# Kernel optimization log

Measured on AMD Instinct MI355X. Metric: run time of the kernel, lower is better.

The kernel has to match this reference:

```python
import jax, jax.numpy as jnp
import numpy as np

BATCH = 4096
IN_F = 1024
OUT_F = 1024
GRID_SIZE = 8
SPLINE_ORDER = 3
SCALE_SPLINE = 1.0


def setup_inputs() -> dict:
    key = jax.random.key(0)
    kx, kb, ks = jax.random.split(key, 3)
    # inputs live on the spline domain [-1, 1]
    x = jax.random.uniform(kx, (BATCH, IN_F), jnp.float32, -1.0, 1.0)
    # kaiming_uniform_(a=sqrt(5)) on (out,in) -> U(-1/sqrt(in), 1/sqrt(in))
    bound = 1.0 / float(np.sqrt(IN_F))
    base_weight = jax.random.uniform(kb, (OUT_F, IN_F), jnp.float32, -bound, bound)
    # normal(mean=0, std=0.1), (out, in, grid_size + spline_order)
    spline_weight = 0.1 * jax.random.normal(ks, (OUT_F, IN_F, GRID_SIZE + SPLINE_ORDER), jnp.float32)
    # uniform knot vector with spacing h = 2/grid_size over [-1,1], extended by
    # spline_order knots on each side so Cox-de Boor yields grid_size+spline_order bases
    h = 2.0 / GRID_SIZE
    grid = jnp.arange(-SPLINE_ORDER, GRID_SIZE + SPLINE_ORDER + 1, dtype=jnp.float32) * h - 1.0
    return {"x": x, "base_weight": base_weight, "spline_weight": spline_weight, "grid": grid}


def b_spline_basis(x, grid, k):
    # x: (batch, in), grid: (grid_size + 2k + 1,) shared across (out, in) pairs
    xe = x[..., None]  # (b, i, 1)
    # degree-0: indicator of knot interval -> (b, i, grid_size + 2k)
    basis = ((xe >= grid[:-1]) & (xe < grid[1:])).astype(x.dtype)
    for d in range(1, k + 1):  # Cox-de Boor recursion up to degree k
        left_denom = grid[d:-1] - grid[:-(d + 1)]
        right_denom = grid[d + 1:] - grid[1:-d]
        left_denom = jnp.where(left_denom > 0, left_denom, 1.0)
        right_denom = jnp.where(right_denom > 0, right_denom, 1.0)
        basis = ((xe - grid[:-(d + 1)]) / left_denom * basis[..., :-1]
                 + (grid[d + 1:] - xe) / right_denom * basis[..., 1:])
    return basis  # (b, i, grid_size + k)


def reference(x, base_weight, spline_weight, grid):
    base_output = x @ base_weight.T  # (b, out)
    basis = b_spline_basis(x, grid, SPLINE_ORDER)  # (b, i, L), L = grid_size + k
    # grid is identical for every (out, in) pair, so the per-(o,i) basis of the
    # original collapses to a per-i basis; einsum 'bil,oil->bo' is the same math.
    spline_output = jnp.einsum('bil,oil->bo', basis, spline_weight)
    return base_output + SCALE_SPLINE * spline_output
```

## Files before the change

### kernel.cpp

```cpp
#include <hip/hip_runtime.h>
#include <hip/hip_bf16.h>
#include <cstdint>

#define BATCH 4096
#define INF   1024
#define OUTF  1024
#define LCH   12
#define KTOT  (INF*LCH)
#define BM    256
#define BN    256
#define BK    48
#define NT    64
#define THREADS 512
#define TSZ   (6*256*8)

#define WTT_BYTES ((size_t)OUTF * KTOT * 2)
#define PART_FLOATS ((size_t)BATCH * OUTF)
#define PQ_U32   (PART_FLOATS / 2)
#define P_BYTES  ((size_t)4 * PQ_U32 * 4)
#define OUT_BYTES (PART_FLOATS * 4)

typedef __bf16 bf16x8 __attribute__((ext_vector_type(8)));
typedef float  f32x16 __attribute__((ext_vector_type(16)));
typedef unsigned long long ull;
typedef unsigned short us;

struct alignas(16) U2 { ull x, y; };

__device__ __forceinline__ us f2bf(float f) {
  unsigned int u = __builtin_bit_cast(unsigned int, f);
  u += 0x7FFFu + ((u >> 16) & 1u);
  return (us)(u >> 16);
}

__device__ __forceinline__ void async_copy16(const void* g, void* l) {
  __builtin_amdgcn_global_load_lds(
      (const __attribute__((address_space(1))) unsigned int*)g,
      (__attribute__((address_space(3))) unsigned int*)l,
      16, 0, 0);
}

#define PIPE_BARRIER() do {                                        \
  asm volatile("s_waitcnt vmcnt(4) lgkmcnt(0)" ::: "memory");      \
  __builtin_amdgcn_sched_barrier(0);                               \
  __builtin_amdgcn_s_barrier();                                    \
  __builtin_amdgcn_sched_barrier(0);                               \
} while (0)

__device__ __forceinline__ void basis12(float xx, ull W[3]) {
  float u  = fmaf(xx, 4.0f, 7.0f);
  float fm = floorf(u);
  int   mi = (int)fm;
  float t  = u - fm;
  float s  = 1.0f - t;
  float t2 = t * t, t3 = t2 * t;
  float w0 = (s * s * s) * (1.0f / 6.0f);
  float w3 = t3 * (1.0f / 6.0f);
  float w1 = fmaf(0.5f, t3, 2.0f / 3.0f) - t2;
  float w2 = 1.0f - w0 - w1 - w3;
  int ls = mi - 3;
  ull W64 = (ull)f2bf(w0)
          | ((ull)f2bf(w1) << 16)
          | ((ull)f2bf(w2) << 32)
          | ((ull)f2bf(w3) << 48);
  int sh = ls << 4;
  int a  = sh & 63;
  ull lop  = W64 << a;
  ull hip_ = a ? (W64 >> (64 - a)) : 0ull;
  W[0] = (sh < 64) ? lop : 0ull;
  W[1] = (sh < 64) ? hip_ : lop;
  W[2] = ((sh < 64) ? 0ull : hip_) | ((ull)f2bf(xx) << 48);
}

__global__ __launch_bounds__(256) void kan_build_wtT(
    const float* __restrict__ sw,
    const float* __restrict__ bw,
    us* __restrict__ WtT)
{
  int t   = blockIdx.x * 256 + threadIdx.x;
  int col = t & 255;
  int q   = t >> 8;
  int fp  = q & 1;
  int ktG = (q >> 1) & 255;
  int bn  = q >> 9;
  int o   = bn * 256 + col;
  int i0  = ktG * 4 + fp * 2;

  const float2* s2 = reinterpret_cast<const float2*>(
      sw + (size_t)(o * 1024 + i0) * 11);
  float2 sv[11];
#pragma unroll
  for (int l = 0; l < 11; ++l) sv[l] = s2[l];
  float2 bv = *reinterpret_cast<const float2*>(bw + (size_t)o * 1024 + i0);

  us v[24];
#pragma unroll
  for (int l = 0; l < 11; ++l) {
    int m0 = l;
    int m1 = 11 + l;
    float f0 = (m0 & 1) ? sv[m0 >> 1].y : sv[m0 >> 1].x;
    float f1 = (m1 & 1) ? sv[m1 >> 1].y : sv[m1 >> 1].x;
    v[l]      = f2bf(f0);
    v[12 + l] = f2bf(f1);
  }
  v[11] = f2bf(bv.x);
  v[23] = f2bf(bv.y);

  int g0 = fp * 3;
  us* base = WtT + (size_t)(bn * 256 + ktG) * (6 * 256 * 8);
  U2* p = reinterpret_cast<U2*>(base);
#pragma unroll
  for (int j = 0; j < 3; ++j) {
    U2 u;
    const us* w = v + j * 8;
    u.x = (ull)w[0] | ((ull)w[1] << 16) | ((ull)w[2] << 32) | ((ull)w[3] << 48);
    u.y = (ull)w[4] | ((ull)w[5] << 16) | ((ull)w[6] << 32) | ((ull)w[7] << 48);
    p[(g0 + j) * 256 + col] = u;
  }
}

#define BASIS2(XV, W0_,W1_,W2_,W3_,W4_,W5_) do {                         \
  {                                                                      \
    float xx = (XV).x;                                                   \
    float u_  = fmaf(xx, 4.0f, 7.0f);                                    \
    float fm_ = floorf(u_);                                              \
    int   mi_ = (int)fm_;                                                \
    float t_  = u_ - fm_;                                                \
    float s_  = 1.0f - t_;                                               \
    float t2_ = t_ * t_, t3_ = t2_ * t_;                                 \
    float w0_ = (s_ * s_ * s_) * (1.0f / 6.0f);                          \
    float w3_ = t3_ * (1.0f / 6.0f);                                     \
    float w1_ = fmaf(0.5f, t3_, 2.0f / 3.0f) - t2_;                      \
    float w2_ = 1.0f - w0_ - w1_ - w3_;                                  \
    unsigned int p01_, p23_;                                             \
    asm("v_cvt_pk_bf16_f32 %0, %1, %2" : "=v"(p01_) : "v"(w0_), "v"(w1_)); \
    asm("v_cvt_pk_bf16_f32 %0, %1, %2" : "=v"(p23_) : "v"(w2_), "v"(w3_)); \
    ull W64_ = (ull)p01_ | ((ull)p23_ << 32);                            \
    int sh_ = (mi_ - 3) << 4;                                            \
    int a_  = sh_ & 63;                                                  \
    ull lo_ = W64_ << a_;                                                \
    ull hi_ = a_ ? (W64_ >> (64 - a_)) : 0ull;                           \
    W0_ = (sh_ < 64) ? lo_ : 0ull;                                       \
    W1_ = (sh_ < 64) ? hi_ : lo_;                                        \
    W2_ = ((sh_ < 64) ? 0ull : hi_) | ((ull)f2bf(xx) << 48);             \
  }                                                                      \
  {                                                                      \
    float xx = (XV).y;                                                   \
    float u_  = fmaf(xx, 4.0f, 7.0f);                                    \
    float fm_ = floorf(u_);                                              \
    int   mi_ = (int)fm_;                                                \
    float t_  = u_ - fm_;                                                \
    float s_  = 1.0f - t_;                                               \
    float t2_ = t_ * t_, t3_ = t2_ * t_;                                 \
    float w0_ = (s_ * s_ * s_) * (1.0f / 6.0f);                          \
    float w3_ = t3_ * (1.0f / 6.0f);                                     \
    float w1_ = fmaf(0.5f, t3_, 2.0f / 3.0f) - t2_;                      \
    float w2_ = 1.0f - w0_ - w1_ - w3_;                                  \
    unsigned int p01_, p23_;                                             \
    asm("v_cvt_pk_bf16_f32 %0, %1, %2" : "=v"(p01_) : "v"(w0_), "v"(w1_)); \
    asm("v_cvt_pk_bf16_f32 %0, %1, %2" : "=v"(p23_) : "v"(w2_), "v"(w3_)); \
    ull W64_ = (ull)p01_ | ((ull)p23_ << 32);                            \
    int sh_ = (mi_ - 3) << 4;                                            \
    int a_  = sh_ & 63;                                                  \
    ull lo_ = W64_ << a_;                                                \
    ull hi_ = a_ ? (W64_ >> (64 - a_)) : 0ull;                           \
    W3_ = (sh_ < 64) ? lo_ : 0ull;                                       \
    W4_ = (sh_ < 64) ? hi_ : lo_;                                        \
    W5_ = ((sh_ < 64) ? 0ull : hi_) | ((ull)f2bf(xx) << 48);             \
  }                                                                      \
} while (0)

__global__ __launch_bounds__(THREADS, 2) void kan_gemm(
    const float* __restrict__ x,
    const us* __restrict__ WtT,
    unsigned int* __restrict__ P)
{
  __shared__ alignas(16) us smem[5 * TSZ];

  const int tid  = threadIdx.x;
  const int lane = tid & 63;
  const int wid  = tid >> 6;
  const int wm   = (wid >> 2) * 128;
  const int wn   = (wid & 3) * 64;
  const int lo   = lane & 31;
  const int lh   = lane >> 5;
  const int b    = (int)blockIdx.x;
  const int bn   = b & 3;
  const int kq   = (b >> 2) & 3;
  const int bm   = b >> 4;

  const int r   = tid & 255;
  const int fp  = tid >> 8;
  const int g0A = fp * 3;
  const float* xrow = x + (size_t)(bm * BM + r) * INF + kq * 256 + fp * 2;

  us* Acur = smem;
  us* Aalt = smem + TSZ;
  us* Bcur = smem + 2 * TSZ;
  us* Bnxt = smem + 3 * TSZ;
  us* Bnn  = smem + 4 * TSZ;

  f32x16 acc[4][2] = {};

  auto stageB = [&](int c, us* Bd) {
    const int ktG = kq * NT + c;
    const us* base = WtT + (size_t)(bn * 256 + ktG) * (6 * 256 * 8);
#pragma unroll
    for (int j = 0; j < 3; ++j) {
      int s = wid * 3 + j;
      int g = s >> 2, h = s & 3;
      async_copy16(base + g * 2048 + h * 512 + lane * 8,
                   Bd + g * 2048 + h * 512);
    }
  };

#define WRITEW(AD, W0_,W1_,W2_,W3_,W4_,W5_) do {                   \
    U2* p_ = reinterpret_cast<U2*>(AD);                            \
    U2 u0_; u0_.x = W0_; u0_.y = W1_;                              \
    U2 u1_; u1_.x = W2_; u1_.y = W3_;                              \
    U2 u2_; u2_.x = W4_; u2_.y = W5_;                              \
    p_[(g0A + 0) * 256 + r] = u0_;                                 \
    p_[(g0A + 1) * 256 + r] = u1_;                                 \
    p_[(g0A + 2) * 256 + r] = u2_;                                 \
  } while (0)

#define READK(S, A0,A1,A2,A3,B0,B1) do {                           \
    const int kk_ = (S) * 2 + lh;                                  \
    A0 = *reinterpret_cast<const bf16x8*>(&Acur[(kk_ * 256 + wm +  0 + lo) * 8]); \
    A1 = *reinterpret_cast<const bf16x8*>(&Acur[(kk_ * 256 + wm + 32 + lo) * 8]); \
    A2 = *reinterpret_cast<const bf16x8*>(&Acur[(kk_ * 256 + wm + 64 + lo) * 8]); \
    A3 = *reinterpret_cast<const bf16x8*>(&Acur[(kk_ * 256 + wm + 96 + lo) * 8]); \
    B0 = *reinterpret_cast<const bf16x8*>(&Bcur[(kk_ * 256 + wn +  0 + lo) * 8]); \
    B1 = *reinterpret_cast<const bf16x8*>(&Bcur[(kk_ * 256 + wn + 32 + lo) * 8]); \
  } while (0)

#define MFMAK(A0,A1,A2,A3,B0,B1) do {                              \
    acc[0][0] = __builtin_amdgcn_mfma_f32_32x32x16_bf16(A0, B0, acc[0][0], 0, 0, 0); \
    acc[0][1] = __builtin_amdgcn_mfma_f32_32x32x16_bf16(A0, B1, acc[0][1], 0, 0, 0); \
    acc[1][0] = __builtin_amdgcn_mfma_f32_32x32x16_bf16(A1, B0, acc[1][0], 0, 0, 0); \
    acc[1][1] = __builtin_amdgcn_mfma_f32_32x32x16_bf16(A1, B1, acc[1][1], 0, 0, 0); \
    acc[2][0] = __builtin_amdgcn_mfma_f32_32x32x16_bf16(A2, B0, acc[2][0], 0, 0, 0); \
    acc[2][1] = __builtin_amdgcn_mfma_f32_32x32x16_bf16(A2, B1, acc[2][1], 0, 0, 0); \
    acc[3][0] = __builtin_amdgcn_mfma_f32_32x32x16_bf16(A3, B0, acc[3][0], 0, 0, 0); \
    acc[3][1] = __builtin_amdgcn_mfma_f32_32x32x16_bf16(A3, B1, acc[3][1], 0, 0, 0); \
  } while (0)

  {
    float2 x0 = *reinterpret_cast<const float2*>(xrow);
    ull W0, W1, W2, W3, W4, W5;
    BASIS2(x0, W0, W1, W2, W3, W4, W5);
    WRITEW(Acur, W0, W1, W2, W3, W4, W5);
    stageB(0, Bcur);
    stageB(1, Bnxt);
  }
  float2 xa = *reinterpret_cast<const float2*>(xrow + 4);
  PIPE_BARRIER();

  for (int c = 0; c < NT; ++c) {
    const int cf = (c + 2 < NT) ? (c + 2) : (NT - 1);

    float2 xb = *reinterpret_cast<const float2*>(xrow + cf * 4);
    stageB(cf, Bnn);

    ull W0, W1, W2, W3, W4, W5;
    bf16x8 a00, a01, a02, a03, b00, b01;
    bf16x8 a10, a11, a12, a13, b10, b11;
    bf16x8 a20, a21, a22, a23, b20, b21;

    READK(0, a00, a01, a02, a03, b00, b01);
    BASIS2(xa, W0, W1, W2, W3, W4, W5);
    READK(1, a10, a11, a12, a13, b10, b11);
    MFMAK(a00, a01, a02, a03, b00, b01);
    READK(2, a20, a21, a22, a23, b20, b21);
    MFMAK(a10, a11, a12, a13, b10, b11);
    __builtin_amdgcn_sched_barrier(0);
    WRITEW(Aalt, W0, W1, W2, W3, W4, W5);
    MFMAK(a20, a21, a22, a23, b20, b21);

    PIPE_BARRIER();

    us* t = Bcur; Bcur = Bnxt; Bnxt = Bnn; Bnn = t;
    t = Acur; Acur = Aalt; Aalt = t;
    xa = xb;
  }

  asm volatile("s_waitcnt vmcnt(0) lgkmcnt(0)" ::: "memory");

  unsigned int* dst = P + (size_t)kq * PQ_U32;
  const int ubase = bn * 128 + (wn >> 1) + lo;
#pragma unroll
  for (int f = 0; f < 4; ++f) {
#pragma unroll
    for (int rr = 0; rr < 16; ++rr) {
      int row = bm * BM + wm + f * 32 + (rr & 3) + 8 * (rr >> 2) + 4 * lh;
      unsigned int pk;
      asm("v_cvt_pk_bf16_f32 %0, %1, %2"
          : "=v"(pk) : "v"(acc[f][0][rr]), "v"(acc[f][1][rr]));
      dst[(size_t)row * 512 + ubase] = pk;
    }
  }
}

__global__ __launch_bounds__(256) void kan_reduce4p(
    float* __restrict__ out, const uint4* __restrict__ P)
{
  size_t i = (size_t)blockIdx.x * 256 + threadIdx.x;
  const size_t Q = PQ_U32 / 4;
  uint4 a = P[i], b = P[i + Q], c = P[i + 2 * Q], d = P[i + 3 * Q];

  size_t u0  = i * 4;
  size_t row = u0 >> 9;
  int ur  = (int)(u0 & 511);
  int pq  = ur >> 7;
  int sub = (ur >> 5) & 3;
  int lo0 = ur & 31;
  int col0 = pq * 256 + sub * 64 + lo0;

  float4 vlo, vhi;
  {
    unsigned int ua[4] = {a.x, a.y, a.z, a.w};
    unsigned int ub[4] = {b.x, b.y, b.z, b.w};
    unsigned int uc[4] = {c.x, c.y, c.z, c.w};
    unsigned int ud[4] = {d.x, d.y, d.z, d.w};
    float* plo = &vlo.x;
    float* phi = &vhi.x;
#pragma unroll
    for (int j = 0; j < 4; ++j) {
      float la = __builtin_bit_cast(float, ua[j] << 16);
      float lb = __builtin_bit_cast(float, ub[j] << 16);
      float lc = __builtin_bit_cast(float, uc[j] << 16);
      float ld = __builtin_bit_cast(float, ud[j] << 16);
      float ha = __builtin_bit_cast(float, ua[j] & 0xffff0000u);
      float hb = __builtin_bit_cast(float, ub[j] & 0xffff0000u);
      float hc = __builtin_bit_cast(float, uc[j] & 0xffff0000u);
      float hd = __builtin_bit_cast(float, ud[j] & 0xffff0000u);
      plo[j] = (la + lb) + (lc + ld);
      phi[j] = (ha + hb) + (hc + hd);
    }
  }
  *reinterpret_cast<float4*>(out + row * 1024 + col0)      = vlo;
  *reinterpret_cast<float4*>(out + row * 1024 + col0 + 32) = vhi;
}

#define FB_BUFSZ (6*128*8)

__global__ __launch_bounds__(256) void kan_build_wt(
    const float* __restrict__ sw, const float* __restrict__ bw,
    us* __restrict__ Wt)
{
  int idx = blockIdx.x * 256 + threadIdx.x;
  int o = idx >> 10;
  int i = idx & 1023;
  const float* s = sw + (size_t)(o * 1024 + i) * 11;
  us v[12];
#pragma unroll
  for (int l = 0; l < 11; ++l) v[l] = f2bf(s[l]);
  v[11] = f2bf(bw[o * 1024 + i]);
  us* d = Wt + (size_t)o * KTOT + i * 12;
  *reinterpret_cast<ushort4*>(d + 0) = make_ushort4(v[0], v[1], v[2],  v[3]);
  *reinterpret_cast<ushort4*>(d + 4) = make_ushort4(v[4], v[5], v[6],  v[7]);
  *reinterpret_cast<ushort4*>(d + 8) = make_ushort4(v[8], v[9], v[10], v[11]);
}

__global__ __launch_bounds__(512, 4) void kan_gemm_fb(
    const float* __restrict__ x, const us* __restrict__ Wt,
    float* __restrict__ out)
{
  __shared__ alignas(16) us smem[5 * FB_BUFSZ];
  const int tid  = threadIdx.x;
  const int lane = tid & 63;
  const int wid  = tid >> 6;
  const int wm   = (wid >> 2) * 64;
  const int wn   = (wid & 3) * 32;
  const int lo   = lane & 31;
  const int lh   = lane >> 5;
  const int idx  = (int)blockIdx.x;
  const int bn   = idx & 7;
  const int kh   = (idx >> 3) & 1;
  const int bm   = idx >> 4;
  const bool builder = (tid < 256);
  const bool stager  = (wid >= 4);
  const int ab  = tid & 127;
  const int ai0 = ((tid >> 7) & 1) << 1;
  const float* xrow = x + (size_t)(bm * 128 + ab) * INF + kh * 512 + ai0;
  const size_t kbase = (size_t)kh * (KTOT / 2);

  us* Bcur = smem;            us* Bnxt = smem + FB_BUFSZ;
  us* Bnn  = smem + 2 * FB_BUFSZ;
  us* Acur = smem + 3 * FB_BUFSZ; us* Aalt = smem + 4 * FB_BUFSZ;
  f32x16 acc[2] = {};

  auto stageB = [&](int c, us* Bd) {
    const int wq = wid - 4;
#pragma unroll
    for (int qq = 0; qq < 3; ++qq) {
      int G  = (wq * 3 + qq) * 64 + lane;
      int kk = G >> 7;
      int oo = G & 127;
      const us* src = Wt + (size_t)(bn * 128 + oo) * KTOT + kbase + c * 48 + kk * 8;
      async_copy16(src, Bd + (wq * 3 + qq) * 512);
    }
  };
  auto buildA = [&](float2 xv, us* Ad) {
    ull W[6];
    basis12(xv.x, W + 0);
    basis12(xv.y, W + 3);
    U2* p = reinterpret_cast<U2*>(Ad);
    const int g0 = (ai0 >> 1) * 3;
    U2 u0; u0.x = W[0]; u0.y = W[1];
    U2 u1; u1.x = W[2]; u1.y = W[3];
    U2 u2; u2.x = W[4]; u2.y = W[5];
    p[(g0 + 0) * 128 + ab] = u0;
    p[(g0 + 1) * 128 + ab] = u1;
    p[(g0 + 2) * 128 + ab] = u2;
  };

  float2 xa = make_float2(0.f, 0.f);
  if (builder) {
    float2 x0v = *reinterpret_cast<const float2*>(xrow);
    buildA(x0v, Acur);
    xa = *reinterpret_cast<const float2*>(xrow + 4);
  }
  if (stager) { stageB(0, Bcur); stageB(1, Bnxt); }
  asm volatile("s_waitcnt vmcnt(3) lgkmcnt(0)" ::: "memory");
  __builtin_amdgcn_s_barrier();

  for (int c = 0; c < 128; ++c) {
    int cf = (c + 2 < 128) ? (c + 2) : 127;
    float2 xb = xa;
    if (builder) {
      xb = *reinterpret_cast<const float2*>(xrow + cf * 4);
      buildA(xa, Aalt);
    }
    if (stager) stageB(cf, Bnn);
#pragma unroll
    for (int s = 0; s < 3; ++s) {
      const int kk = s * 2 + lh;
      bf16x8 a0 = *reinterpret_cast<const bf16x8*>(&Acur[(kk * 128 + wm + lo) * 8]);
      bf16x8 a1 = *reinterpret_cast<const bf16x8*>(&Acur[(kk * 128 + wm + 32 + lo) * 8]);
      bf16x8 b0 = *reinterpret_cast<const bf16x8*>(&Bcur[(kk * 128 + wn + lo) * 8]);
      acc[0] = __builtin_amdgcn_mfma_f32_32x32x16_bf16(a0, b0, acc[0], 0, 0, 0);
      acc[1] = __builtin_amdgcn_mfma_f32_32x32x16_bf16(a1, b0, acc[1], 0, 0, 0);
    }
    asm volatile("s_waitcnt vmcnt(3) lgkmcnt(0)" ::: "memory");
    __builtin_amdgcn_s_barrier();
    us* t = Bcur; Bcur = Bnxt; Bnxt = Bnn; Bnn = t;
    t = Acur; Acur = Aalt; Aalt = t;
    xa = xb;
  }
  asm volatile("s_waitcnt vmcnt(0) lgkmcnt(0)" ::: "memory");
#pragma unroll
  for (int mf = 0; mf < 2; ++mf)
#pragma unroll
    for (int r2 = 0; r2 < 16; ++r2) {
      int row = bm * 128 + wm + mf * 32 + (r2 & 3) + 8 * (r2 >> 2) + 4 * lh;
      atomicAdd(out + (size_t)row * OUTF + bn * 128 + wn + lo, acc[mf][r2]);
    }
}

extern "C" void kernel_launch(void* const* d_in, const int* in_sizes, int n_in,
                              void* d_out, int out_size, void* d_ws, size_t ws_size,
                              hipStream_t stream) {
  const float* x  = (const float*)d_in[0];
  const float* bw = (const float*)d_in[1];
  const float* sw = (const float*)d_in[2];
  float* out = (float*)d_out;

  if (ws_size >= WTT_BYTES + P_BYTES) {
    us* WtT = (us*)d_ws;
    unsigned int* P = (unsigned int*)((char*)d_ws + WTT_BYTES);
    kan_build_wtT<<<2048, 256, 0, stream>>>(sw, bw, WtT);
    kan_gemm<<<256, THREADS, 0, stream>>>(x, WtT, P);
    kan_reduce4p<<<(int)(PQ_U32 / 4 / 256), 256, 0, stream>>>(
        out, (const uint4*)P);
  } else if (ws_size >= WTT_BYTES) {
    us* Wt = (us*)d_ws;
    kan_build_wt<<<(OUTF * INF) / 256, 256, 0, stream>>>(sw, bw, Wt);
    hipMemsetAsync(d_out, 0, OUT_BYTES, stream);
    kan_gemm_fb<<<512, 512, 0, stream>>>(x, Wt, out);
  }
}
```

Before: 146.6 us.

## Halve GEMM N-tile to 128 and double-buffer B to raise occupancy

Shrinks the GEMM block tile from 256x256 to 256x128 and the per-wave tile to 64x64. B staging drops from triple to double buffering, which cuts LDS and accumulator registers and lets four blocks per CU be requested. The grid doubles to 512 blocks, with the weight pre-layout and reduce column mapping updated to match. In exchange, the spline basis for each A tile is now computed twice (once per N-half), B-tile loads are issued only one step ahead, and each loaded A element gets less reuse.

```diff
diff --git a/kernel.cpp b/kernel.cpp
--- a/kernel.cpp
+++ b/kernel.cpp
@@ -8,11 +8,12 @@
 #define LCH   12
 #define KTOT  (INF*LCH)
 #define BM    256
-#define BN    256
+#define BN    128
 #define BK    48
 #define NT    64
 #define THREADS 512
-#define TSZ   (6*256*8)
+#define ASZ   (6*256*8)
+#define BSZ   (6*128*8)
 
 #define WTT_BYTES ((size_t)OUTF * KTOT * 2)
 #define PART_FLOATS ((size_t)BATCH * OUTF)
@@ -41,7 +42,7 @@
 }
 
 #define PIPE_BARRIER() do {                                        \
-  asm volatile("s_waitcnt vmcnt(4) lgkmcnt(0)" ::: "memory");      \
+  asm volatile("s_waitcnt vmcnt(1) lgkmcnt(0)" ::: "memory");      \
   __builtin_amdgcn_sched_barrier(0);                               \
   __builtin_amdgcn_s_barrier();                                    \
   __builtin_amdgcn_sched_barrier(0);                               \
@@ -78,12 +79,12 @@
     us* __restrict__ WtT)
 {
   int t   = blockIdx.x * 256 + threadIdx.x;
-  int col = t & 255;
-  int q   = t >> 8;
+  int col = t & 127;
+  int q   = t >> 7;
   int fp  = q & 1;
   int ktG = (q >> 1) & 255;
   int bn  = q >> 9;
-  int o   = bn * 256 + col;
+  int o   = bn * 128 + col;
   int i0  = ktG * 4 + fp * 2;
 
   const float2* s2 = reinterpret_cast<const float2*>(
@@ -107,7 +108,7 @@
   v[23] = f2bf(bv.y);
 
   int g0 = fp * 3;
-  us* base = WtT + (size_t)(bn * 256 + ktG) * (6 * 256 * 8);
+  us* base = WtT + (size_t)(bn * 256 + ktG) * (6 * 128 * 8);
   U2* p = reinterpret_cast<U2*>(base);
 #pragma unroll
   for (int j = 0; j < 3; ++j) {
@@ -115,7 +116,7 @@
     const us* w = v + j * 8;
     u.x = (ull)w[0] | ((ull)w[1] << 16) | ((ull)w[2] << 32) | ((ull)w[3] << 48);
     u.y = (ull)w[4] | ((ull)w[5] << 16) | ((ull)w[6] << 32) | ((ull)w[7] << 48);
-    p[(g0 + j) * 256 + col] = u;
+    p[(g0 + j) * 128 + col] = u;
   }
 }
 
@@ -170,24 +171,24 @@
   }                                                                      \
 } while (0)
 
-__global__ __launch_bounds__(THREADS, 2) void kan_gemm(
+__global__ __launch_bounds__(THREADS, 4) void kan_gemm(
     const float* __restrict__ x,
     const us* __restrict__ WtT,
     unsigned int* __restrict__ P)
 {
-  __shared__ alignas(16) us smem[5 * TSZ];
+  __shared__ alignas(16) us smem[2 * ASZ + 2 * BSZ];
 
   const int tid  = threadIdx.x;
   const int lane = tid & 63;
   const int wid  = tid >> 6;
-  const int wm   = (wid >> 2) * 128;
-  const int wn   = (wid & 3) * 64;
+  const int wm   = (wid >> 1) * 64;
+  const int wn   = (wid & 1) * 64;
   const int lo   = lane & 31;
   const int lh   = lane >> 5;
   const int b    = (int)blockIdx.x;
-  const int bn   = b & 3;
-  const int kq   = (b >> 2) & 3;
-  const int bm   = b >> 4;
+  const int bn   = b & 7;
+  const int kq   = (b >> 3) & 3;
+  const int bm   = b >> 5;
 
   const int r   = tid & 255;
   const int fp  = tid >> 8;
@@ -195,22 +196,23 @@
   const float* xrow = x + (size_t)(bm * BM + r) * INF + kq * 256 + fp * 2;
 
   us* Acur = smem;
-  us* Aalt = smem + TSZ;
-  us* Bcur = smem + 2 * TSZ;
-  us* Bnxt = smem + 3 * TSZ;
-  us* Bnn  = smem + 4 * TSZ;
-
-  f32x16 acc[4][2] = {};
+  us* Aalt = smem + ASZ;
+  us* Bcur = smem + 2 * ASZ;
+  us* Balt = smem + 2 * ASZ + BSZ;
+
+  f32x16 acc[2][2] = {};
 
   auto stageB = [&](int c, us* Bd) {
-    const int ktG = kq * NT + c;
-    const us* base = WtT + (size_t)(bn * 256 + ktG) * (6 * 256 * 8);
-#pragma unroll
-    for (int j = 0; j < 3; ++j) {
-      int s = wid * 3 + j;
-      int g = s >> 2, h = s & 3;
-      async_copy16(base + g * 2048 + h * 512 + lane * 8,
-                   Bd + g * 2048 + h * 512);
+    if (wid < 6) {
+      const int ktG = kq * NT + c;
+      const us* base = WtT + (size_t)(bn * 256 + ktG) * (6 * 128 * 8);
+#pragma unroll
+      for (int j = 0; j < 2; ++j) {
+        int ch = wid * 2 + j;
+        int g = ch >> 1, h = ch & 1;
+        async_copy16(base + g * 1024 + h * 512 + lane * 8,
+                     Bd + g * 1024 + h * 512);
+      }
     }
   };
 
@@ -224,34 +226,27 @@
     p_[(g0A + 2) * 256 + r] = u2_;                                 \
   } while (0)
 
-#define READK(S, A0,A1,A2,A3,B0,B1) do {                           \
+#define READK(S, A0,A1,B0,B1) do {                                 \
     const int kk_ = (S) * 2 + lh;                                  \
     A0 = *reinterpret_cast<const bf16x8*>(&Acur[(kk_ * 256 + wm +  0 + lo) * 8]); \
     A1 = *reinterpret_cast<const bf16x8*>(&Acur[(kk_ * 256 + wm + 32 + lo) * 8]); \
-    A2 = *reinterpret_cast<const bf16x8*>(&Acur[(kk_ * 256 + wm + 64 + lo) * 8]); \
-    A3 = *reinterpret_cast<const bf16x8*>(&Acur[(kk_ * 256 + wm + 96 + lo) * 8]); \
-    B0 = *reinterpret_cast<const bf16x8*>(&Bcur[(kk_ * 256 + wn +  0 + lo) * 8]); \
-    B1 = *reinterpret_cast<const bf16x8*>(&Bcur[(kk_ * 256 + wn + 32 + lo) * 8]); \
+    B0 = *reinterpret_cast<const bf16x8*>(&Bcur[(kk_ * 128 + wn +  0 + lo) * 8]); \
+    B1 = *reinterpret_cast<const bf16x8*>(&Bcur[(kk_ * 128 + wn + 32 + lo) * 8]); \
   } while (0)
 
-#define MFMAK(A0,A1,A2,A3,B0,B1) do {                              \
+#define MFMAK(A0,A1,B0,B1) do {                                    \
     acc[0][0] = __builtin_amdgcn_mfma_f32_32x32x16_bf16(A0, B0, acc[0][0], 0, 0, 0); \
     acc[0][1] = __builtin_amdgcn_mfma_f32_32x32x16_bf16(A0, B1, acc[0][1], 0, 0, 0); \
     acc[1][0] = __builtin_amdgcn_mfma_f32_32x32x16_bf16(A1, B0, acc[1][0], 0, 0, 0); \
     acc[1][1] = __builtin_amdgcn_mfma_f32_32x32x16_bf16(A1, B1, acc[1][1], 0, 0, 0); \
-    acc[2][0] = __builtin_amdgcn_mfma_f32_32x32x16_bf16(A2, B0, acc[2][0], 0, 0, 0); \
-    acc[2][1] = __builtin_amdgcn_mfma_f32_32x32x16_bf16(A2, B1, acc[2][1], 0, 0, 0); \
-    acc[3][0] = __builtin_amdgcn_mfma_f32_32x32x16_bf16(A3, B0, acc[3][0], 0, 0, 0); \
-    acc[3][1] = __builtin_amdgcn_mfma_f32_32x32x16_bf16(A3, B1, acc[3][1], 0, 0, 0); \
   } while (0)
 
+  stageB(0, Bcur);
   {
     float2 x0 = *reinterpret_cast<const float2*>(xrow);
     ull W0, W1, W2, W3, W4, W5;
     BASIS2(x0, W0, W1, W2, W3, W4, W5);
     WRITEW(Acur, W0, W1, W2, W3, W4, W5);
-    stageB(0, Bcur);
-    stageB(1, Bnxt);
   }
   float2 xa = *reinterpret_cast<const float2*>(xrow + 4);
   PIPE_BARRIER();
@@ -259,27 +254,27 @@
   for (int c = 0; c < NT; ++c) {
     const int cf = (c + 2 < NT) ? (c + 2) : (NT - 1);
 
+    stageB(c + 1 < NT ? c + 1 : NT - 1, Balt);
     float2 xb = *reinterpret_cast<const float2*>(xrow + cf * 4);
-    stageB(cf, Bnn);
 
     ull W0, W1, W2, W3, W4, W5;
-    bf16x8 a00, a01, a02, a03, b00, b01;
-    bf16x8 a10, a11, a12, a13, b10, b11;
-    bf16x8 a20, a21, a22, a23, b20, b21;
-
-    READK(0, a00, a01, a02, a03, b00, b01);
+    bf16x8 a00, a01, b00, b01;
+    bf16x8 a10, a11, b10, b11;
+    bf16x8 a20, a21, b20, b21;
+
+    READK(0, a00, a01, b00, b01);
     BASIS2(xa, W0, W1, W2, W3, W4, W5);
-    READK(1, a10, a11, a12, a13, b10, b11);
-    MFMAK(a00, a01, a02, a03, b00, b01);
-    READK(2, a20, a21, a22, a23, b20, b21);
-    MFMAK(a10, a11, a12, a13, b10, b11);
+    READK(1, a10, a11, b10, b11);
+    MFMAK(a00, a01, b00, b01);
+    READK(2, a20, a21, b20, b21);
+    MFMAK(a10, a11, b10, b11);
     __builtin_amdgcn_sched_barrier(0);
     WRITEW(Aalt, W0, W1, W2, W3, W4, W5);
-    MFMAK(a20, a21, a22, a23, b20, b21);
+    MFMAK(a20, a21, b20, b21);
 
     PIPE_BARRIER();
 
-    us* t = Bcur; Bcur = Bnxt; Bnxt = Bnn; Bnn = t;
+    us* t = Bcur; Bcur = Balt; Balt = t;
     t = Acur; Acur = Aalt; Aalt = t;
     xa = xb;
   }
@@ -287,9 +282,9 @@
   asm volatile("s_waitcnt vmcnt(0) lgkmcnt(0)" ::: "memory");
 
   unsigned int* dst = P + (size_t)kq * PQ_U32;
-  const int ubase = bn * 128 + (wn >> 1) + lo;
-#pragma unroll
-  for (int f = 0; f < 4; ++f) {
+  const int ubase = bn * 64 + (wn >> 1) + lo;
+#pragma unroll
+  for (int f = 0; f < 2; ++f) {
 #pragma unroll
     for (int rr = 0; rr < 16; ++rr) {
       int row = bm * BM + wm + f * 32 + (rr & 3) + 8 * (rr >> 2) + 4 * lh;
@@ -310,11 +305,8 @@
 
   size_t u0  = i * 4;
   size_t row = u0 >> 9;
-  int ur  = (int)(u0 & 511);
-  int pq  = ur >> 7;
-  int sub = (ur >> 5) & 3;
-  int lo0 = ur & 31;
-  int col0 = pq * 256 + sub * 64 + lo0;
+  int ur   = (int)(u0 & 511);
+  int col0 = (ur >> 6) * 128 + ((ur >> 5) & 1) * 64 + (ur & 31);
 
   float4 vlo, vhi;
   {
@@ -470,7 +462,7 @@
     us* WtT = (us*)d_ws;
     unsigned int* P = (unsigned int*)((char*)d_ws + WTT_BYTES);
     kan_build_wtT<<<2048, 256, 0, stream>>>(sw, bw, WtT);
-    kan_gemm<<<256, THREADS, 0, stream>>>(x, WtT, P);
+    kan_gemm<<<512, THREADS, 0, stream>>>(x, WtT, P);
     kan_reduce4p<<<(int)(PQ_U32 / 4 / 256), 256, 0, stream>>>(
         out, (const uint4*)P);
   } else if (ws_size >= WTT_BYTES) {
```

After: 140.7 us, median of 2. -4.0%, faster.
